# Performance work log

Hardware: AMD Instinct MI355X
Metric: run time of the kernel (lower is better)

Reference implementation:

```python
import jax, jax.numpy as jnp
from jax import lax
import numpy as np

H = 16   # num_heads
K = 31   # kernel_size
P = 15   # padding_l (left padding for 'same')


def setup_inputs() -> dict:
    key = jax.random.key(0)
    k1, k2, k3 = jax.random.split(key, 3)
    T, B, C = 2048, 32, 512
    x = jax.random.normal(k1, (T, B, C), dtype=jnp.float32)
    # xavier-uniform-ish init for (H, 1, K)
    limit = float(np.sqrt(6.0 / (1 + K)))
    weight = jax.random.uniform(k2, (H, 1, K), dtype=jnp.float32, minval=-limit, maxval=limit)
    bias = jnp.zeros((C,), dtype=jnp.float32)
    return {"x": x, "weight": weight, "bias": bias}


def reference(x, weight, bias):
    # x: (T, B, C); weight: (H, 1, K); bias: (C,)
    T, B, C = x.shape
    R = C // H  # channels per head
    w = weight.reshape(H, K)
    # weight_softmax=True: softmax over kernel dim in fp32, cast back
    w = jax.nn.softmax(w.astype(jnp.float32), axis=1).astype(weight.dtype)
    # expand per-head weights to per-channel depthwise kernel (C, 1, K)
    wc = jnp.repeat(w, R, axis=0)[:, None, :]
    x_bct = jnp.transpose(x, (1, 2, 0))  # (B, C, T)
    # out[b,c,t] = sum_k wc[c,0,k] * x[b,c,t - P + k], zero-padded
    out = lax.conv_general_dilated(
        x_bct, wc,
        window_strides=(1,),
        padding=[(P, K - 1 - P)],
        feature_group_count=C,
        dimension_numbers=("NCH", "OIH", "NCH"),
    )  # (B, C, T)
    out = jnp.transpose(out, (2, 0, 1))  # (T, B, C)
    return out + bias[None, None, :]
```

## Files before the change

kernel.cpp:

```cpp
#include <hip/hip_runtime.h>

#define T_DIM 2048
#define B_DIM 32
#define C_DIM 512
#define H_DIM 16
#define K_DIM 31
#define P_PAD 15
#define TT 32
#define JN (TT + K_DIM - 1)
#define NCOL (B_DIM * C_DIM)

__global__ __launch_bounds__(256, 4)
void lwconv_kernel(const float* __restrict__ x, const float* __restrict__ weight,
                   const float* __restrict__ bias, float* __restrict__ out)
{
    const int wid  = __builtin_amdgcn_readfirstlane((int)(threadIdx.x >> 6));
    const int lane = threadIdx.x & 63;
    const int gw   = blockIdx.x * 4 + wid;
    const int h    = gw & (H_DIM - 1);
    const int bp   = (gw >> 4) & 15;
    const int tblk = gw >> 8;
    const int c    = (h << 5) | (lane & 31);
    const int b    = (bp << 1) | (lane >> 5);
    const int col  = b * C_DIM + c;

    float w[K_DIM];
    float m = -3.4e38f;
    #pragma unroll
    for (int k = 0; k < K_DIM; ++k) { w[k] = weight[h * K_DIM + k]; m = fmaxf(m, w[k]); }
    float s = 0.f;
    #pragma unroll
    for (int k = 0; k < K_DIM; ++k) { w[k] = __expf(w[k] - m); s += w[k]; }
    const float inv = 1.f / s;
    unsigned int ws[K_DIM];
    #pragma unroll
    for (int k = 0; k < K_DIM; ++k)
        ws[k] = __builtin_amdgcn_readfirstlane(__float_as_uint(w[k] * inv));

    const float bv = bias[c];
    const int tb = tblk * TT;
    const float* xp = x + col;
    float*       op = out + col;

    float acc[TT];
    #pragma unroll
    for (int i = 0; i < TT; ++i) acc[i] = bv;

    #pragma unroll
    for (int j = 0; j < JN; ++j) {
        const int t  = tb - P_PAD + j;
        int tc = t < 0 ? 0 : (t >= T_DIM ? T_DIM - 1 : t);
        float v = xp[(size_t)tc * NCOL];
        if (t < 0 || t >= T_DIM) v = 0.f;
        const int ilo = (j - (K_DIM - 1)) > 0 ? (j - (K_DIM - 1)) : 0;
        const int ihi = j < (TT - 1) ? j : (TT - 1);
        #pragma unroll
        for (int i = ilo; i <= ihi; ++i)
            acc[i] = fmaf(__uint_as_float(ws[j - i]), v, acc[i]);
    }

    #pragma unroll
    for (int i = 0; i < TT; ++i)
        op[(size_t)(tb + i) * NCOL] = acc[i];
}

extern "C" void kernel_launch(void* const* d_in, const int* in_sizes, int n_in,
                              void* d_out, int out_size, void* d_ws, size_t ws_size,
                              hipStream_t stream) {
    const float* x      = (const float*)d_in[0];
    const float* weight = (const float*)d_in[1];
    const float* bias   = (const float*)d_in[2];
    float* out = (float*)d_out;
    dim3 grid(H_DIM * 16 * (T_DIM / TT) / 4);
    dim3 block(256);
    lwconv_kernel<<<grid, block, 0, stream>>>(x, weight, bias, out);
}
```

Baseline: 52.42 us.

## Stage input time tiles in LDS via direct global-to-LDS loads

Each block now loads a 96-row by 64-column tile of x straight into shared memory with global_load_lds, then four waves each compute 16 output timesteps for 64 channels from LDS. Previously every wave read its 62-row halo directly from global memory, so about twice as much input was fetched per output. The new layout also drops the per-element boundary check for interior tiles and raises the occupancy hint. In exchange it adds a block-wide barrier and roughly 24 KB of LDS per block, and each thread carries fewer accumulators.

After: 62.40 us. 19.0% more time.

```diff
diff --git a/kernel.cpp b/kernel.cpp
--- a/kernel.cpp
+++ b/kernel.cpp
@@ -6,62 +6,99 @@
 #define H_DIM 16
 #define K_DIM 31
 #define P_PAD 15
-#define TT 32
-#define JN (TT + K_DIM - 1)
+#define TBLK 64
+#define ROWS 96
+#define CT 64
 #define NCOL (B_DIM * C_DIM)
 
-__global__ __launch_bounds__(256, 4)
+__global__ __launch_bounds__(256, 6)
 void lwconv_kernel(const float* __restrict__ x, const float* __restrict__ weight,
                    const float* __restrict__ bias, float* __restrict__ out)
 {
-    const int wid  = __builtin_amdgcn_readfirstlane((int)(threadIdx.x >> 6));
-    const int lane = threadIdx.x & 63;
-    const int gw   = blockIdx.x * 4 + wid;
-    const int h    = gw & (H_DIM - 1);
-    const int bp   = (gw >> 4) & 15;
-    const int tblk = gw >> 8;
-    const int c    = (h << 5) | (lane & 31);
-    const int b    = (bp << 1) | (lane >> 5);
-    const int col  = b * C_DIM + c;
+    __shared__ float smem[ROWS * CT];
 
-    float w[K_DIM];
+    const int tid  = threadIdx.x;
+    const int w    = tid >> 6;
+    const int lane = tid & 63;
+    const int bid  = blockIdx.x;
+    const int tt   = bid & 31;
+    const int ct   = bid >> 5;
+    const int colbase = ct * CT;
+    const int t0   = tt * TBLK;
+
+    {
+        const int rbase = w * 24;
+        const float* src0 = x + colbase + ((lane & 15) << 2);
+        #pragma unroll
+        for (int l = 0; l < 6; ++l) {
+            const int r = rbase + (l << 2) + (lane >> 4);
+            int tg = t0 - P_PAD + r;
+            tg = tg < 0 ? 0 : (tg >= T_DIM ? T_DIM - 1 : tg);
+            const float* src = src0 + (size_t)tg * NCOL;
+            __builtin_amdgcn_global_load_lds(
+                (const __attribute__((address_space(1))) void*)src,
+                (__attribute__((address_space(3))) void*)&smem[(rbase + (l << 2)) * CT],
+                16, 0, 0);
+        }
+    }
+
+    const int hloc = w & 1;
+    const int tq   = ((w >> 1) << 1) | (lane >> 5);
+    const int cl   = (hloc << 5) | (lane & 31);
+    const int hg   = ((ct & 7) << 1) | hloc;
+
+    float wt[K_DIM];
     float m = -3.4e38f;
     #pragma unroll
-    for (int k = 0; k < K_DIM; ++k) { w[k] = weight[h * K_DIM + k]; m = fmaxf(m, w[k]); }
+    for (int k = 0; k < K_DIM; ++k) { wt[k] = weight[hg * K_DIM + k]; m = fmaxf(m, wt[k]); }
     float s = 0.f;
     #pragma unroll
-    for (int k = 0; k < K_DIM; ++k) { w[k] = __expf(w[k] - m); s += w[k]; }
+    for (int k = 0; k < K_DIM; ++k) { wt[k] = __expf(wt[k] - m); s += wt[k]; }
     const float inv = 1.f / s;
     unsigned int ws[K_DIM];
     #pragma unroll
     for (int k = 0; k < K_DIM; ++k)
-        ws[k] = __builtin_amdgcn_readfirstlane(__float_as_uint(w[k] * inv));
+        ws[k] = __builtin_amdgcn_readfirstlane(__float_as_uint(wt[k] * inv));
 
-    const float bv = bias[c];
-    const int tb = tblk * TT;
-    const float* xp = x + col;
-    float*       op = out + col;
+    asm volatile("s_waitcnt vmcnt(0)" ::: "memory");
+    __syncthreads();
 
-    float acc[TT];
+    const float bv = bias[((ct & 7) << 6) + cl];
+    float acc[16];
     #pragma unroll
-    for (int i = 0; i < TT; ++i) acc[i] = bv;
+    for (int i = 0; i < 16; ++i) acc[i] = bv;
 
-    #pragma unroll
-    for (int j = 0; j < JN; ++j) {
-        const int t  = tb - P_PAD + j;
-        int tc = t < 0 ? 0 : (t >= T_DIM ? T_DIM - 1 : t);
-        float v = xp[(size_t)tc * NCOL];
-        if (t < 0 || t >= T_DIM) v = 0.f;
-        const int ilo = (j - (K_DIM - 1)) > 0 ? (j - (K_DIM - 1)) : 0;
-        const int ihi = j < (TT - 1) ? j : (TT - 1);
+    const float* sp = &smem[(tq << 4) * CT + cl];
+    const int tbase = t0 + (tq << 4) - P_PAD;
+
+    if (tt == 0 || tt == 31) {
         #pragma unroll
-        for (int i = ilo; i <= ihi; ++i)
-            acc[i] = fmaf(__uint_as_float(ws[j - i]), v, acc[i]);
+        for (int j = 0; j < 46; ++j) {
+            float v = sp[j * CT];
+            const int t = tbase + j;
+            if (t < 0 || t >= T_DIM) v = 0.f;
+            const int ilo = (j - 30) > 0 ? (j - 30) : 0;
+            const int ihi = j < 15 ? j : 15;
+            #pragma unroll
+            for (int i = ilo; i <= ihi; ++i)
+                acc[i] = fmaf(__uint_as_float(ws[j - i]), v, acc[i]);
+        }
+    } else {
+        #pragma unroll
+        for (int j = 0; j < 46; ++j) {
+            float v = sp[j * CT];
+            const int ilo = (j - 30) > 0 ? (j - 30) : 0;
+            const int ihi = j < 15 ? j : 15;
+            #pragma unroll
+            for (int i = ilo; i <= ihi; ++i)
+                acc[i] = fmaf(__uint_as_float(ws[j - i]), v, acc[i]);
+        }
     }
 
+    float* op = out + (size_t)(t0 + (tq << 4)) * NCOL + colbase + cl;
     #pragma unroll
-    for (int i = 0; i < TT; ++i)
-        op[(size_t)(tb + i) * NCOL] = acc[i];
+    for (int i = 0; i < 16; ++i)
+        op[(size_t)i * NCOL] = acc[i];
 }
 
 extern "C" void kernel_launch(void* const* d_in, const int* in_sizes, int n_in,
@@ -71,7 +108,7 @@
     const float* weight = (const float*)d_in[1];
     const float* bias   = (const float*)d_in[2];
     float* out = (float*)d_out;
-    dim3 grid(H_DIM * 16 * (T_DIM / TT) / 4);
+    dim3 grid((NCOL / CT) * (T_DIM / TBLK));
     dim3 block(256);
     lwconv_kernel<<<grid, block, 0, stream>>>(x, weight, bias, out);
 }
```

## Vectorize to float2 columns, halve time tile, split boundary path

Applied to the files above, without the earlier changes.

Each lane now processes two adjacent channels via float2 loads/stores, with 16 batch×channel-pairs per wave and a time tile of 16 instead of 32. Interior tiles skip the clamp/zero logic, and loads are software-pipelined one step ahead. The smaller time tile raises redundant halo reads of the input, relying on cache to absorb them.

Result: slower. 72.87 us (+39.0%).

```diff
diff --git a/kernel.cpp b/kernel.cpp
--- a/kernel.cpp
+++ b/kernel.cpp
@@ -6,23 +6,25 @@
 #define H_DIM 16
 #define K_DIM 31
 #define P_PAD 15
-#define TT 32
-#define JN (TT + K_DIM - 1)
-#define NCOL (B_DIM * C_DIM)
+#define TP 16
+#define JN (TP + K_DIM - 1)
+#define NC2 (B_DIM * C_DIM / 2)
+
+typedef float f32x2 __attribute__((ext_vector_type(2)));
 
 __global__ __launch_bounds__(256, 4)
-void lwconv_kernel(const float* __restrict__ x, const float* __restrict__ weight,
-                   const float* __restrict__ bias, float* __restrict__ out)
+void lwconv_kernel(const f32x2* __restrict__ x2, const float* __restrict__ weight,
+                   const float* __restrict__ bias, f32x2* __restrict__ out2)
 {
     const int wid  = __builtin_amdgcn_readfirstlane((int)(threadIdx.x >> 6));
     const int lane = threadIdx.x & 63;
     const int gw   = blockIdx.x * 4 + wid;
     const int h    = gw & (H_DIM - 1);
-    const int bp   = (gw >> 4) & 15;
-    const int tblk = gw >> 8;
-    const int c    = (h << 5) | (lane & 31);
-    const int b    = (bp << 1) | (lane >> 5);
-    const int col  = b * C_DIM + c;
+    const int bq   = (gw >> 4) & 7;
+    const int tseg = gw >> 7;
+    const int c2   = lane & 15;
+    const int bl   = lane >> 4;
+    const int b    = (bq << 2) | bl;
 
     float w[K_DIM];
     float m = -3.4e38f;
@@ -37,41 +39,73 @@
     for (int k = 0; k < K_DIM; ++k)
         ws[k] = __builtin_amdgcn_readfirstlane(__float_as_uint(w[k] * inv));
 
-    const float bv = bias[c];
-    const int tb = tblk * TT;
-    const float* xp = x + col;
-    float*       op = out + col;
+    const int col2 = b * (C_DIM / 2) + (h << 4) + c2;
+    const f32x2 bv = ((const f32x2*)bias)[(h << 4) + c2];
+    const int tb = tseg * TP;
+    const f32x2* xp = x2 + col2;
+    f32x2*       op = out2 + col2;
 
-    float acc[TT];
+    float aA[TP], aB[TP];
     #pragma unroll
-    for (int i = 0; i < TT; ++i) acc[i] = bv;
+    for (int i = 0; i < TP; ++i) { aA[i] = bv[0]; aB[i] = bv[1]; }
+
+#define FMAS(J, V)                                                        \
+    {                                                                     \
+        const int ilo = ((J) - (K_DIM - 1)) > 0 ? ((J) - (K_DIM - 1)) : 0;\
+        const int ihi = (J) < (TP - 1) ? (J) : (TP - 1);                  \
+        _Pragma("unroll")                                                 \
+        for (int i = ilo; i <= ihi; ++i) {                                \
+            const float wk = __uint_as_float(ws[(J) - i]);                \
+            aA[i] = fmaf(wk, (V)[0], aA[i]);                              \
+            aB[i] = fmaf(wk, (V)[1], aB[i]);                              \
+        }                                                                 \
+    }
+
+    if (tseg == 0 || tseg == (T_DIM / TP) - 1) {
+        f32x2 vc;
+        {
+            int t = tb - P_PAD;
+            int tc = t < 0 ? 0 : (t >= T_DIM ? T_DIM - 1 : t);
+            vc = xp[(size_t)tc * NC2];
+            if (t < 0 || t >= T_DIM) { vc[0] = 0.f; vc[1] = 0.f; }
+        }
+        #pragma unroll
+        for (int j = 0; j < JN - 1; ++j) {
+            int t = tb - P_PAD + j + 1;
+            int tc = t < 0 ? 0 : (t >= T_DIM ? T_DIM - 1 : t);
+            f32x2 vn = xp[(size_t)tc * NC2];
+            if (t < 0 || t >= T_DIM) { vn[0] = 0.f; vn[1] = 0.f; }
+            FMAS(j, vc);
+            vc = vn;
+        }
+        FMAS(JN - 1, vc);
+    } else {
+        f32x2 vc = xp[(size_t)(tb - P_PAD) * NC2];
+        #pragma unroll
+        for (int j = 0; j < JN - 1; ++j) {
+            f32x2 vn = xp[(size_t)(tb - P_PAD + j + 1) * NC2];
+            FMAS(j, vc);
+            vc = vn;
+        }
+        FMAS(JN - 1, vc);
+    }
+#undef FMAS
 
     #pragma unroll
-    for (int j = 0; j < JN; ++j) {
-        const int t  = tb - P_PAD + j;
-        int tc = t < 0 ? 0 : (t >= T_DIM ? T_DIM - 1 : t);
-        float v = xp[(size_t)tc * NCOL];
-        if (t < 0 || t >= T_DIM) v = 0.f;
-        const int ilo = (j - (K_DIM - 1)) > 0 ? (j - (K_DIM - 1)) : 0;
-        const int ihi = j < (TT - 1) ? j : (TT - 1);
-        #pragma unroll
-        for (int i = ilo; i <= ihi; ++i)
-            acc[i] = fmaf(__uint_as_float(ws[j - i]), v, acc[i]);
+    for (int i = 0; i < TP; ++i) {
+        f32x2 r; r[0] = aA[i]; r[1] = aB[i];
+        op[(size_t)(tb + i) * NC2] = r;
     }
-
-    #pragma unroll
-    for (int i = 0; i < TT; ++i)
-        op[(size_t)(tb + i) * NCOL] = acc[i];
 }
 
 extern "C" void kernel_launch(void* const* d_in, const int* in_sizes, int n_in,
                               void* d_out, int out_size, void* d_ws, size_t ws_size,
                               hipStream_t stream) {
-    const float* x      = (const float*)d_in[0];
+    const f32x2* x2     = (const f32x2*)d_in[0];
     const float* weight = (const float*)d_in[1];
     const float* bias   = (const float*)d_in[2];
-    float* out = (float*)d_out;
-    dim3 grid(H_DIM * 16 * (T_DIM / TT) / 4);
+    f32x2* out2 = (f32x2*)d_out;
+    dim3 grid(H_DIM * 8 * (T_DIM / TP) / 4);
     dim3 block(256);
-    lwconv_kernel<<<grid, block, 0, stream>>>(x, weight, bias, out);
+    lwconv_kernel<<<grid, block, 0, stream>>>(x2, weight, bias, out2);
 }
```
